# Kernel tuning notes

Measured on AMD Instinct MI355X. Metric: run time of the kernel, lower is better.

The kernel has to match this reference:

```python
import jax, jax.numpy as jnp
import numpy as np

B, T, C, H = 4, 2048, 1024, 16
HS = C // H  # head_size = 64
FF = 4 * C   # 4096
EPS = 1e-5


def _layernorm(x, g, b):
    mu = jnp.mean(x, axis=-1, keepdims=True)
    var = jnp.mean(jnp.square(x - mu), axis=-1, keepdims=True)
    return (x - mu) * jax.lax.rsqrt(var + EPS) * g + b


def setup_inputs() -> dict:
    key = jax.random.key(0)
    ks = jax.random.split(key, 12)
    s_in = 1.0 / np.sqrt(C)
    s_ff = 1.0 / np.sqrt(FF)
    return {
        "x": jax.random.normal(ks[0], (B, T, C), jnp.float32),
        # per-head projection weights stacked: [H, C, HS]
        "Wq": jax.random.normal(ks[1], (H, C, HS), jnp.float32) * s_in,
        "Wk": jax.random.normal(ks[2], (H, C, HS), jnp.float32) * s_in,
        "Wv": jax.random.normal(ks[3], (H, C, HS), jnp.float32) * s_in,
        "Wo": jax.random.normal(ks[4], (C, C), jnp.float32) * s_in,
        "bo": jnp.zeros((C,), jnp.float32),
        "g1": jnp.ones((C,), jnp.float32),
        "b1": jnp.zeros((C,), jnp.float32),
        "g2": jnp.ones((C,), jnp.float32),
        "b2": jnp.zeros((C,), jnp.float32),
        "W1": jax.random.normal(ks[5], (C, FF), jnp.float32) * s_in,
        "bf1": jnp.zeros((FF,), jnp.float32),
        "W2": jax.random.normal(ks[6], (FF, C), jnp.float32) * s_ff,
        "bf2": jnp.zeros((C,), jnp.float32),
    }


def reference(x, Wq, Wk, Wv, Wo, bo, g1, b1, g2, b2, W1, bf1, W2, bf2):
    # pre-norm
    h = _layernorm(x, g1, b1)                       # [B,T,C]
    q = jnp.einsum('btc,hcd->bhtd', h, Wq)          # [B,H,T,HS]
    k = jnp.einsum('btc,hcd->bhtd', h, Wk)
    v = jnp.einsum('btc,hcd->bhtd', h, Wv)
    w = jnp.einsum('bhtd,bhsd->bhts', q, k) * (HS ** -0.5)  # [B,H,T,S]
    mask = jnp.tril(jnp.ones((T, T), bool))          # causal tril
    w = jnp.where(mask[None, None], w, -jnp.inf)
    # NB: original code softmaxes over dim=1 of [B,T,T], i.e. the QUERY axis
    w = jax.nn.softmax(w, axis=-2)
    o = jnp.einsum('bhts,bhsd->bhtd', w, v)          # [B,H,T,HS]
    o = jnp.transpose(o, (0, 2, 1, 3)).reshape(B, T, C)  # concat heads
    x = x + o @ Wo + bo                              # residual 1 (dropout=0)
    f = _layernorm(x, g2, b2)
    ff = jax.nn.relu(f @ W1 + bf1) @ W2 + bf2        # FFN (dropout=0)
    return x + ff
```

## Files before the change

### kernel.cpp

```cpp
#include <hip/hip_runtime.h>
#include <hip/hip_bf16.h>


#define T_SEQ 2048
#define SCALE2 0.1803368801f

typedef __attribute__((ext_vector_type(8))) short short8;
typedef __attribute__((ext_vector_type(4))) float f32x4;

typedef __attribute__((address_space(1))) unsigned int g_u32;
typedef __attribute__((address_space(3))) unsigned int l_u32;

__device__ __forceinline__ unsigned short f2bf(float f) {
  __hip_bfloat16 h = __float2bfloat16(f);
  union { __hip_bfloat16 h; unsigned short u; } x; x.h = h;
  return x.u;
}
__device__ __forceinline__ float bf2f(unsigned short u) {
  union { unsigned u; float f; } x; x.u = (unsigned)u << 16;
  return x.f;
}

__device__ __forceinline__ void g2lds16(const void* g, void* l) {
  __builtin_amdgcn_global_load_lds((g_u32*)g, (l_u32*)l, 16, 0, 0);
}

__device__ __forceinline__ int xcd_swz(int flat, int nwg) {
  if ((nwg & 7) != 0) return flat;
  return (flat & 7) * (nwg >> 3) + (flat >> 3);
}

template <int EPI, int BN>
__global__ __launch_bounds__(512, 2) void gemm256(
    const unsigned short* __restrict__ A, const unsigned short* __restrict__ Bt,
    int M, int N, int K,
    unsigned short* __restrict__ out16, float* __restrict__ outF,
    const float* __restrict__ bias, const float* __restrict__ resid) {
  constexpr int WN = BN / 4;
  constexpr int FN = WN / 16;
  constexpr int NL = 4 + (BN * 8) / 512;
  extern __shared__ unsigned short lds[];
  unsigned short* ldsA = lds;
  unsigned short* ldsB = lds + 2 * 16384;
  const int tid = threadIdx.x, lane = tid & 63, wid = tid >> 6;
  const int wm = wid >> 2, wn = wid & 3;
  const int nx = gridDim.x;
  const int flat = blockIdx.y * nx + blockIdx.x;
  const int swz = xcd_swz(flat, nx * gridDim.y);
  const int mBase = (swz / nx) * 256, nBase = (swz % nx) * BN;

  f32x4 acc[8][FN];
#pragma unroll
  for (int i = 0; i < 8; ++i)
#pragma unroll
    for (int j = 0; j < FN; ++j)
#pragma unroll
      for (int e = 0; e < 4; ++e) acc[i][j][e] = 0.f;

  auto stage = [&](int buf, int kt) {
    const int k0 = kt << 6;
#pragma unroll
    for (int it = 0; it < 4; ++it) {
      int g = it * 512 + tid;
      int row = g >> 3, colL = g & 7;
      int col = colL ^ (row & 7);
      g2lds16(A + ((size_t)(mBase + row) * K + k0 + col * 8),
              &ldsA[buf * 16384 + (it * 512 + wid * 64) * 8]);
    }
#pragma unroll
    for (int it = 0; it < (BN * 8) / 512; ++it) {
      int g = it * 512 + tid;
      int row = g >> 3, colL = g & 7;
      int col = colL ^ (row & 7);
      g2lds16(Bt + ((size_t)(nBase + row) * K + k0 + col * 8),
              &ldsB[buf * (BN * 64) + (it * 512 + wid * 64) * 8]);
    }
  };

  const int nKT = K >> 6;
  stage(0, 0);
  asm volatile("s_waitcnt vmcnt(0)" ::: "memory");
  __builtin_amdgcn_sched_barrier(0);
  __builtin_amdgcn_s_barrier();
  __builtin_amdgcn_sched_barrier(0);
  if (nKT > 1) stage(1, 1);

  int cur = 0;
  for (int kt = 0; kt < nKT; ++kt) {
    short8 bf[FN][2];
#pragma unroll
    for (int fn = 0; fn < FN; ++fn)
#pragma unroll
      for (int ks = 0; ks < 2; ++ks) {
        int r = wn * WN + fn * 16 + (lane & 15);
        int c = (ks * 4 + (lane >> 4)) ^ (r & 7);
        bf[fn][ks] = *(const short8*)&ldsB[cur * (BN * 64) + r * 64 + c * 8];
      }
#pragma unroll
    for (int q = 0; q < 4; ++q) {
      short8 af[2][2];
#pragma unroll
      for (int mf = 0; mf < 2; ++mf)
#pragma unroll
        for (int ks = 0; ks < 2; ++ks) {
          int r = wm * 128 + q * 32 + mf * 16 + (lane & 15);
          int c = (ks * 4 + (lane >> 4)) ^ (r & 7);
          af[mf][ks] = *(const short8*)&ldsA[cur * 16384 + r * 64 + c * 8];
        }
      __builtin_amdgcn_s_setprio(1);
#pragma unroll
      for (int mf = 0; mf < 2; ++mf)
#pragma unroll
        for (int fn = 0; fn < FN; ++fn)
#pragma unroll
          for (int ks = 0; ks < 2; ++ks)
            acc[q * 2 + mf][fn] = __builtin_amdgcn_mfma_f32_16x16x32_bf16(
                af[mf][ks], bf[fn][ks], acc[q * 2 + mf][fn], 0, 0, 0);
      __builtin_amdgcn_s_setprio(0);
    }
    if (kt + 1 < nKT) {
      asm volatile("s_waitcnt lgkmcnt(0)" ::: "memory");
      __builtin_amdgcn_sched_barrier(0);
      __builtin_amdgcn_s_barrier();
      __builtin_amdgcn_sched_barrier(0);
      if (kt + 2 < nKT) {
        stage(cur, kt + 2);
        asm volatile("s_waitcnt vmcnt(%0)" ::"n"(NL) : "memory");
      } else {
        asm volatile("s_waitcnt vmcnt(0)" ::: "memory");
      }
      __builtin_amdgcn_sched_barrier(0);
      __builtin_amdgcn_s_barrier();
      __builtin_amdgcn_sched_barrier(0);
    }
    cur ^= 1;
  }

#pragma unroll
  for (int am = 0; am < 8; ++am)
#pragma unroll
    for (int fn = 0; fn < FN; ++fn) {
      int col = nBase + wn * WN + fn * 16 + (lane & 15);
      int row0 = mBase + wm * 128 + am * 16 + ((lane >> 4) << 2);
      if (EPI == 0) {
#pragma unroll
        for (int r = 0; r < 4; ++r)
          out16[(size_t)(row0 + r) * N + col] = f2bf(acc[am][fn][r]);
      } else if (EPI == 1) {
        float bv = bias[col];
#pragma unroll
        for (int r = 0; r < 4; ++r) {
          size_t idx = (size_t)(row0 + r) * N + col;
          outF[idx] = acc[am][fn][r] + bv + resid[idx];
        }
      } else {
        float bv = bias[col];
#pragma unroll
        for (int r = 0; r < 4; ++r)
          out16[(size_t)(row0 + r) * N + col] =
              f2bf(fmaxf(acc[am][fn][r] + bv, 0.f));
      }
    }
}

__global__ __launch_bounds__(256) void ln_bf16(
    const float* __restrict__ x, const float* __restrict__ gw,
    const float* __restrict__ bw, unsigned short* __restrict__ out) {
  __shared__ float red[8];
  const int row = blockIdx.x, tid = threadIdx.x;
  const float4 v = ((const float4*)(x + (size_t)row * 1024))[tid];
  float s = v.x + v.y + v.z + v.w;
  float q = v.x * v.x + v.y * v.y + v.z * v.z + v.w * v.w;
#pragma unroll
  for (int off = 32; off >= 1; off >>= 1) {
    s += __shfl_down(s, off);
    q += __shfl_down(q, off);
  }
  const int lane = tid & 63, wid = tid >> 6;
  if (lane == 0) { red[wid] = s; red[4 + wid] = q; }
  __syncthreads();
  float S = red[0] + red[1] + red[2] + red[3];
  float Q = red[4] + red[5] + red[6] + red[7];
  float mu = S * (1.f / 1024.f);
  float var = Q * (1.f / 1024.f) - mu * mu;
  float rs = rsqrtf(var + 1e-5f);
  int c = tid * 4;
  ushort4 ov;
  ov.x = f2bf((v.x - mu) * rs * gw[c + 0] + bw[c + 0]);
  ov.y = f2bf((v.y - mu) * rs * gw[c + 1] + bw[c + 1]);
  ov.z = f2bf((v.z - mu) * rs * gw[c + 2] + bw[c + 2]);
  ov.w = f2bf((v.w - mu) * rs * gw[c + 3] + bw[c + 3]);
  *(ushort4*)&out[(size_t)row * 1024 + c] = ov;
}

__global__ __launch_bounds__(256) void pack_qkv(
    const float* __restrict__ Wq, const float* __restrict__ Wk,
    const float* __restrict__ Wv, unsigned short* __restrict__ out) {
  __shared__ float tile[64 * 65];
  const int tid = threadIdx.x;
  const float* W = (blockIdx.z == 0) ? Wq : (blockIdx.z == 1) ? Wk : Wv;
  const int h = blockIdx.y, r0 = blockIdx.x * 64;
#pragma unroll
  for (int it = 0; it < 4; ++it) {
    int e4 = it * 256 + tid;
    int r = e4 >> 4, c4 = e4 & 15;
    float4 v = *(const float4*)&W[((size_t)h * 1024 + r0 + r) * 64 + c4 * 4];
    tile[r * 65 + c4 * 4 + 0] = v.x;
    tile[r * 65 + c4 * 4 + 1] = v.y;
    tile[r * 65 + c4 * 4 + 2] = v.z;
    tile[r * 65 + c4 * 4 + 3] = v.w;
  }
  __syncthreads();
#pragma unroll
  for (int it = 0; it < 4; ++it) {
    int e4 = it * 256 + tid;
    int d = e4 >> 4, r4 = e4 & 15;
    ushort4 ov;
    ov.x = f2bf(tile[(r4 * 4 + 0) * 65 + d]);
    ov.y = f2bf(tile[(r4 * 4 + 1) * 65 + d]);
    ov.z = f2bf(tile[(r4 * 4 + 2) * 65 + d]);
    ov.w = f2bf(tile[(r4 * 4 + 3) * 65 + d]);
    *(ushort4*)&out[(size_t)(blockIdx.z * 1024 + h * 64 + d) * 1024 + r0 +
                    r4 * 4] = ov;
  }
}

__global__ __launch_bounds__(256) void transpose_cast(
    const float* __restrict__ in, unsigned short* __restrict__ out, int R,
    int C) {
  __shared__ float tile[64 * 65];
  const int tid = threadIdx.x;
  const int r0 = blockIdx.x * 64, c0 = blockIdx.y * 64;
#pragma unroll
  for (int it = 0; it < 4; ++it) {
    int e4 = it * 256 + tid;
    int r = e4 >> 4, c4 = e4 & 15;
    float4 v = *(const float4*)&in[(size_t)(r0 + r) * C + c0 + c4 * 4];
    tile[r * 65 + c4 * 4 + 0] = v.x;
    tile[r * 65 + c4 * 4 + 1] = v.y;
    tile[r * 65 + c4 * 4 + 2] = v.z;
    tile[r * 65 + c4 * 4 + 3] = v.w;
  }
  __syncthreads();
#pragma unroll
  for (int it = 0; it < 4; ++it) {
    int e4 = it * 256 + tid;
    int c = e4 >> 4, r4 = e4 & 15;
    ushort4 ov;
    ov.x = f2bf(tile[(r4 * 4 + 0) * 65 + c]);
    ov.y = f2bf(tile[(r4 * 4 + 1) * 65 + c]);
    ov.z = f2bf(tile[(r4 * 4 + 2) * 65 + c]);
    ov.w = f2bf(tile[(r4 * 4 + 3) * 65 + c]);
    *(ushort4*)&out[(size_t)(c0 + c) * R + r0 + r4 * 4] = ov;
  }
}

__global__ __launch_bounds__(256) void vtrans(
    const unsigned short* __restrict__ qkv, const float* __restrict__ lpart,
    unsigned short* __restrict__ vT) {
  __shared__ unsigned short tile[64 * 66];
  const int tid = threadIdx.x;
  const int bh = blockIdx.y, b = bh >> 4, h = bh & 15;
  const int t0 = blockIdx.x * 64;
#pragma unroll
  for (int it = 0; it < 8; ++it) {
    int e2 = it * 256 + tid;
    int r = e2 >> 5, c2 = e2 & 31;
    unsigned v = *(const unsigned*)&qkv[(size_t)(b * T_SEQ + t0 + r) * 3072 +
                                        2048 + h * 64 + c2 * 2];
    float l0 = lpart[(size_t)bh * T_SEQ + t0 + r];
    float l1 = lpart[(size_t)(64 + bh) * T_SEQ + t0 + r];
    float li = 1.f / (l0 + l1);
    unsigned short lo = f2bf(bf2f((unsigned short)(v & 0xffff)) * li);
    unsigned short hi = f2bf(bf2f((unsigned short)(v >> 16)) * li);
    *(unsigned*)&tile[r * 66 + c2 * 2] = (unsigned)lo | ((unsigned)hi << 16);
  }
  __syncthreads();
#pragma unroll
  for (int it = 0; it < 8; ++it) {
    int e2 = it * 256 + tid;
    int d = e2 >> 5, t2 = e2 & 31;
    unsigned short a = tile[(t2 * 2) * 66 + d];
    unsigned short bb = tile[(t2 * 2 + 1) * 66 + d];
    unsigned pk = (unsigned)a | ((unsigned)bb << 16);
    *(unsigned*)&vT[(size_t)(bh * 64 + d) * T_SEQ + t0 + t2 * 2] = pk;
  }
}

__global__ __launch_bounds__(256, 4) void attn_stats(
    const unsigned short* __restrict__ qkv, float* __restrict__ lpart) {
  __shared__ unsigned short qt[4][2][32 * 64];
  __shared__ float redL[4][2][64];
  const int tid = threadIdx.x, lane = tid & 63, w = tid >> 6;
  const int f = xcd_swz(blockIdx.y * 32 + blockIdx.x, 2048);
  const int half = f & 1, px = (f >> 1) & 15, bh = f >> 5;
  const int b = bh >> 4, h = bh & 15;
  const int sxA = px, sxB = 31 - px;
  const int sA = sxA * 64, sB = sxB * 64;
  const int m = half * 4 + w;

  short8 kfA[4][2], kfB[4][2];
#pragma unroll
  for (int fn = 0; fn < 4; ++fn)
#pragma unroll
    for (int ks = 0; ks < 2; ++ks) {
      int d = 1024 + h * 64 + ks * 32 + ((lane >> 4) << 3);
      kfA[fn][ks] = *(const short8*)&qkv[(size_t)(b * T_SEQ + sA + fn * 16 +
                                                  (lane & 15)) * 3072 + d];
      kfB[fn][ks] = *(const short8*)&qkv[(size_t)(b * T_SEQ + sB + fn * 16 +
                                                  (lane & 15)) * 3072 + d];
    }
  float lA[4] = {0.f, 0.f, 0.f, 0.f}, lB[4] = {0.f, 0.f, 0.f, 0.f};

  auto stageQ = [&](int buf, int idx) {
    int t0 = idx * 32;
#pragma unroll
    for (int it = 0; it < 4; ++it) {
      int g = it * 64 + lane;
      int row = g >> 3;
      int col = (g & 7) ^ (row & 7);
      g2lds16(qkv + ((size_t)(b * T_SEQ + t0 + row) * 3072 + h * 64 + col * 8),
              &qt[w][buf][it * 512]);
    }
  };

  auto accum = [&](const short8 (&af)[2], const short8 (&kf)[4][2],
                   float (&lacc)[4], int sBase, int tRow, bool diag) {
    f32x4 sc[4];
#pragma unroll
    for (int fn = 0; fn < 4; ++fn)
#pragma unroll
      for (int e = 0; e < 4; ++e) sc[fn][e] = 0.f;
    __builtin_amdgcn_s_setprio(1);
#pragma unroll
    for (int fn = 0; fn < 4; ++fn)
#pragma unroll
      for (int ks = 0; ks < 2; ++ks)
        sc[fn] = __builtin_amdgcn_mfma_f32_16x16x32_bf16(af[ks], kf[fn][ks],
                                                         sc[fn], 0, 0, 0);
    __builtin_amdgcn_s_setprio(0);
    if (diag) {
#pragma unroll
      for (int fn = 0; fn < 4; ++fn) {
        int s = sBase + fn * 16 + (lane & 15);
        float e0 = (tRow + 0 >= s) ? exp2f(sc[fn][0] * SCALE2) : 0.f;
        float e1 = (tRow + 1 >= s) ? exp2f(sc[fn][1] * SCALE2) : 0.f;
        float e2 = (tRow + 2 >= s) ? exp2f(sc[fn][2] * SCALE2) : 0.f;
        float e3 = (tRow + 3 >= s) ? exp2f(sc[fn][3] * SCALE2) : 0.f;
        lacc[fn] += (e0 + e1) + (e2 + e3);
      }
    } else {
#pragma unroll
      for (int fn = 0; fn < 4; ++fn) {
        float e0 = exp2f(sc[fn][0] * SCALE2);
        float e1 = exp2f(sc[fn][1] * SCALE2);
        float e2 = exp2f(sc[fn][2] * SCALE2);
        float e3 = exp2f(sc[fn][3] * SCALE2);
        lacc[fn] += (e0 + e1) + (e2 + e3);
      }
    }
  };

  const int d0 = 2 * sxA - m;
  const int fi = m + (d0 > 0 ? (((d0 + 7) >> 3) << 3) : 0);
  int cur = 0;
  if (fi < 64) stageQ(0, fi);
  for (int idx = fi; idx < 64; idx += 8, cur ^= 1) {
    if (idx + 8 < 64) {
      stageQ(cur ^ 1, idx + 8);
      asm volatile("s_waitcnt vmcnt(4)" ::: "memory");
    } else {
      asm volatile("s_waitcnt vmcnt(0)" ::: "memory");
    }
    const int t0g = idx * 32;
    const bool doB = idx >= 2 * sxB;
#pragma unroll
    for (int mf = 0; mf < 2; ++mf) {
      short8 af[2];
#pragma unroll
      for (int ks = 0; ks < 2; ++ks) {
        int r = mf * 16 + (lane & 15);
        int c = (ks * 4 + (lane >> 4)) ^ (r & 7);
        af[ks] = *(const short8*)&qt[w][cur][r * 64 + c * 8];
      }
      int tRow = t0g + mf * 16 + ((lane >> 4) << 2);
      accum(af, kfA, lA, sA, tRow, idx <= 2 * sxA + 1);
      if (doB) accum(af, kfB, lB, sB, tRow, idx <= 2 * sxB + 1);
    }
  }
#pragma unroll
  for (int fn = 0; fn < 4; ++fn) {
    lA[fn] += __shfl_down(lA[fn], 32);
    lA[fn] += __shfl_down(lA[fn], 16);
    lB[fn] += __shfl_down(lB[fn], 32);
    lB[fn] += __shfl_down(lB[fn], 16);
  }
  if (lane < 16) {
#pragma unroll
    for (int fn = 0; fn < 4; ++fn) {
      redL[w][0][fn * 16 + lane] = lA[fn];
      redL[w][1][fn * 16 + lane] = lB[fn];
    }
  }
  __syncthreads();
  if (tid < 128) {
    int which = tid >> 6;
    float l = redL[0][which][lane] + redL[1][which][lane] +
              redL[2][which][lane] + redL[3][which][lane];
    int sbase = (which == 0) ? sA : sB;
    lpart[((size_t)half * 64 + bh) * T_SEQ + sbase + lane] = l;
  }
}

__global__ __launch_bounds__(256, 2) void attn_pv(
    const unsigned short* __restrict__ qkv, const unsigned short* __restrict__ vT,
    unsigned short* __restrict__ o) {
  __shared__ unsigned short kbuf[2][64 * 64];
  __shared__ unsigned short vbuf[2][64 * 64];
  __shared__ unsigned short pl[128 * 64];
  const int tid = threadIdx.x, lane = tid & 63, wid = tid >> 6;
  const int f = xcd_swz(blockIdx.y * 8 + blockIdx.x, 512);
  const int bx = f & 7, bh = f >> 3;
  const int b = bh >> 4, h = bh & 15;
  const int tA = bx * 128, tB = (15 - bx) * 128;
  const int nSTA = 2 * bx + 2, nSTB = 32 - 2 * bx;

  short8 qfA[2][2], qfB[2][2];
#pragma unroll
  for (int mf = 0; mf < 2; ++mf)
#pragma unroll
    for (int ks = 0; ks < 2; ++ks) {
      int d = h * 64 + ks * 32 + ((lane >> 4) << 3);
      int rloc = wid * 32 + mf * 16 + (lane & 15);
      qfA[mf][ks] =
          *(const short8*)&qkv[(size_t)(b * T_SEQ + tA + rloc) * 3072 + d];
      qfB[mf][ks] =
          *(const short8*)&qkv[(size_t)(b * T_SEQ + tB + rloc) * 3072 + d];
    }
  f32x4 oaccA[2][4], oaccB[2][4];
#pragma unroll
  for (int i = 0; i < 2; ++i)
#pragma unroll
    for (int j = 0; j < 4; ++j)
#pragma unroll
      for (int e = 0; e < 4; ++e) { oaccA[i][j][e] = 0.f; oaccB[i][j][e] = 0.f; }

  auto stage = [&](int buf, int st) {
#pragma unroll
    for (int it = 0; it < 2; ++it) {
      int g = it * 256 + tid;
      int row = g >> 3, colL = g & 7;
      int col = colL ^ (row & 7);
      g2lds16(qkv + ((size_t)(b * T_SEQ + st * 64 + row) * 3072 + 1024 +
                     h * 64 + col * 8),
              &kbuf[buf][(it * 256 + wid * 64) * 8]);
      g2lds16(vT + ((size_t)(bh * 64 + row) * T_SEQ + st * 64 + col * 8),
              &vbuf[buf][(it * 256 + wid * 64) * 8]);
    }
  };

  auto qkstore = [&](const short8 (&qf)[2][2], int tBase, int s0,
                     bool maskNeeded, int cur) {
    f32x4 sc[4][2];
#pragma unroll
    for (int i = 0; i < 4; ++i)
#pragma unroll
      for (int j = 0; j < 2; ++j)
#pragma unroll
        for (int e = 0; e < 4; ++e) sc[i][j][e] = 0.f;
    __builtin_amdgcn_s_setprio(1);
#pragma unroll
    for (int fn = 0; fn < 4; ++fn)
#pragma unroll
      for (int ks = 0; ks < 2; ++ks) {
        int r = fn * 16 + (lane & 15);
        int c = (ks * 4 + (lane >> 4)) ^ (r & 7);
        short8 kfr = *(const short8*)&kbuf[cur][r * 64 + c * 8];
        sc[fn][0] = __builtin_amdgcn_mfma_f32_16x16x32_bf16(kfr, qf[0][ks],
                                                            sc[fn][0], 0, 0, 0);
        sc[fn][1] = __builtin_amdgcn_mfma_f32_16x16x32_bf16(kfr, qf[1][ks],
                                                            sc[fn][1], 0, 0, 0);
      }
    __builtin_amdgcn_s_setprio(0);
#pragma unroll
    for (int mf = 0; mf < 2; ++mf) {
      int tl = wid * 32 + mf * 16 + (lane & 15);
      int tG = tBase + tl;
#pragma unroll
      for (int fn = 0; fn < 4; ++fn) {
        int sl = fn * 16 + ((lane >> 4) << 2);
        float p0 = exp2f(sc[fn][mf][0] * SCALE2);
        float p1 = exp2f(sc[fn][mf][1] * SCALE2);
        float p2 = exp2f(sc[fn][mf][2] * SCALE2);
        float p3 = exp2f(sc[fn][mf][3] * SCALE2);
        if (maskNeeded) {
          int sG = s0 + sl;
          p0 = (tG >= sG + 0) ? p0 : 0.f;
          p1 = (tG >= sG + 1) ? p1 : 0.f;
          p2 = (tG >= sG + 2) ? p2 : 0.f;
          p3 = (tG >= sG + 3) ? p3 : 0.f;
        }
        uint2 pk;
        pk.x = (unsigned)f2bf(p0) | ((unsigned)f2bf(p1) << 16);
        pk.y = (unsigned)f2bf(p2) | ((unsigned)f2bf(p3) << 16);
        int byteoff = tl * 128 + ((sl * 2) ^ ((tl & 7) << 4));
        *(uint2*)((char*)pl + byteoff) = pk;
      }
    }
  };

  auto pvphase = [&](f32x4 (&oacc)[2][4], int cur) {
    __builtin_amdgcn_s_setprio(1);
#pragma unroll
    for (int ks = 0; ks < 2; ++ks) {
      short8 pa[2];
#pragma unroll
      for (int mf = 0; mf < 2; ++mf) {
        int rowa = wid * 32 + mf * 16 + (lane & 15);
        int kb = ks * 64 + ((lane >> 4) << 4);
        pa[mf] = *(const short8*)((const char*)pl + rowa * 128 +
                                  (kb ^ ((rowa & 7) << 4)));
      }
#pragma unroll
      for (int df = 0; df < 4; ++df) {
        int r = df * 16 + (lane & 15);
        int c = (ks * 4 + (lane >> 4)) ^ (r & 7);
        short8 vb = *(const short8*)&vbuf[cur][r * 64 + c * 8];
        oacc[0][df] = __builtin_amdgcn_mfma_f32_16x16x32_bf16(pa[0], vb,
                                                              oacc[0][df], 0, 0, 0);
        oacc[1][df] = __builtin_amdgcn_mfma_f32_16x16x32_bf16(pa[1], vb,
                                                              oacc[1][df], 0, 0, 0);
      }
    }
    __builtin_amdgcn_s_setprio(0);
  };

  auto bar_lgkm = [&]() {
    asm volatile("s_waitcnt lgkmcnt(0)" ::: "memory");
    __builtin_amdgcn_sched_barrier(0);
    __builtin_amdgcn_s_barrier();
    __builtin_amdgcn_sched_barrier(0);
  };

  stage(0, 0);
  asm volatile("s_waitcnt vmcnt(0)" ::: "memory");
  __builtin_amdgcn_sched_barrier(0);
  __builtin_amdgcn_s_barrier();
  __builtin_amdgcn_sched_barrier(0);

  int cur = 0;
  for (int st = 0; st < nSTB; ++st) {
    const int s0 = st * 64;
    const bool doA = st < nSTA;

    if (st + 1 < nSTB) stage(cur ^ 1, st + 1);

    if (doA) {
      qkstore(qfA, tA, s0, st >= nSTA - 2, cur);
      bar_lgkm();
      pvphase(oaccA, cur);
      bar_lgkm();
    }
    qkstore(qfB, tB, s0, st >= nSTB - 2, cur);
    bar_lgkm();
    pvphase(oaccB, cur);
    asm volatile("s_waitcnt vmcnt(0) lgkmcnt(0)" ::: "memory");
    __builtin_amdgcn_sched_barrier(0);
    __builtin_amdgcn_s_barrier();
    __builtin_amdgcn_sched_barrier(0);
    cur ^= 1;
  }
#pragma unroll
  for (int mf = 0; mf < 2; ++mf)
#pragma unroll
    for (int df = 0; df < 4; ++df) {
      int d = h * 64 + df * 16 + (lane & 15);
      int ra = tA + wid * 32 + mf * 16 + ((lane >> 4) << 2);
      int rb = tB + wid * 32 + mf * 16 + ((lane >> 4) << 2);
#pragma unroll
      for (int r = 0; r < 4; ++r) {
        o[(size_t)(b * T_SEQ + ra + r) * 1024 + d] = f2bf(oaccA[mf][df][r]);
        o[(size_t)(b * T_SEQ + rb + r) * 1024 + d] = f2bf(oaccB[mf][df][r]);
      }
    }
}

extern "C" void kernel_launch(void* const* d_in, const int* in_sizes, int n_in,
                              void* d_out, int out_size, void* d_ws,
                              size_t ws_size, hipStream_t stream) {
  const float* x = (const float*)d_in[0];
  const float* Wq = (const float*)d_in[1];
  const float* Wk = (const float*)d_in[2];
  const float* Wv = (const float*)d_in[3];
  const float* Wo = (const float*)d_in[4];
  const float* bo = (const float*)d_in[5];
  const float* g1 = (const float*)d_in[6];
  const float* b1 = (const float*)d_in[7];
  const float* g2 = (const float*)d_in[8];
  const float* b2 = (const float*)d_in[9];
  const float* W1 = (const float*)d_in[10];
  const float* bf1 = (const float*)d_in[11];
  const float* W2 = (const float*)d_in[12];
  const float* bf2 = (const float*)d_in[13];
  float* out = (float*)d_out;

  char* ws = (char*)d_ws;
  size_t off = 0;
  auto alloc = [&](size_t bytes) {
    char* p = ws + off;
    off += (bytes + 255) & ~(size_t)255;
    return p;
  };
  unsigned short* Wqkv = (unsigned short*)alloc(3072ull * 1024 * 2);
  unsigned short* WoT = (unsigned short*)alloc(1024ull * 1024 * 2);
  unsigned short* W1T = (unsigned short*)alloc(4096ull * 1024 * 2);
  unsigned short* W2T = (unsigned short*)alloc(1024ull * 4096 * 2);
  unsigned short* hbuf = (unsigned short*)alloc(8192ull * 1024 * 2);
  char* regionE = alloc(8192ull * 3072 * 2 + 64ull * 64 * 2048 * 2);
  unsigned short* qkv = (unsigned short*)regionE;
  unsigned short* vT = (unsigned short*)(regionE + 8192ull * 3072 * 2);
  unsigned short* act = (unsigned short*)regionE;
  float* lbuf = (float*)alloc(128ull * 2048 * 4);
  float* x1 = (float*)alloc(8192ull * 1024 * 4);
  unsigned short* fbuf = (unsigned short*)alloc(8192ull * 1024 * 2);
  unsigned short* obuf = hbuf;

  (void)in_sizes; (void)n_in; (void)out_size; (void)ws_size;

  const size_t LDS128 = (2 * 16384 + 2 * 128 * 64) * 2;
  const size_t LDS256 = (2 * 16384 + 2 * 256 * 64) * 2;

  pack_qkv<<<dim3(16, 16, 3), 256, 0, stream>>>(Wq, Wk, Wv, Wqkv);
  transpose_cast<<<dim3(16, 16), 256, 0, stream>>>(Wo, WoT, 1024, 1024);
  transpose_cast<<<dim3(16, 64), 256, 0, stream>>>(W1, W1T, 1024, 4096);
  transpose_cast<<<dim3(64, 16), 256, 0, stream>>>(W2, W2T, 4096, 1024);
  ln_bf16<<<8192, 256, 0, stream>>>(x, g1, b1, hbuf);
  gemm256<0, 128><<<dim3(24, 32), 512, LDS128, stream>>>(
      hbuf, Wqkv, 8192, 3072, 1024, qkv, nullptr, nullptr, nullptr);
  attn_stats<<<dim3(32, 64), 256, 0, stream>>>(qkv, lbuf);
  vtrans<<<dim3(32, 64), 256, 0, stream>>>(qkv, lbuf, vT);
  attn_pv<<<dim3(8, 64), 256, 0, stream>>>(qkv, vT, obuf);
  gemm256<1, 128><<<dim3(8, 32), 512, LDS128, stream>>>(
      obuf, WoT, 8192, 1024, 1024, nullptr, x1, bo, x);
  ln_bf16<<<8192, 256, 0, stream>>>(x1, g2, b2, fbuf);
  gemm256<2, 256><<<dim3(16, 32), 512, LDS256, stream>>>(
      fbuf, W1T, 8192, 4096, 1024, act, nullptr, bf1, nullptr);
  gemm256<1, 128><<<dim3(8, 32), 512, LDS128, stream>>>(
      act, W2T, 8192, 1024, 4096, nullptr, out, bf2, x1);
}
```

Measured before the change: 429.1 us.

## Triple-buffer GEMM LDS pipeline and use 128-wide tiles for FFN1

Moves the GEMM K-loop from double to triple buffering, so two tiles are in flight while one is consumed, and adjusts the vmcnt waits to match. To fit the larger LDS budget, the kernel is fixed to BN=128 and the FFN up-projection drops from 256-wide to 128-wide tiles, which doubles its grid. The aim is to hide global load latency better. In exchange it uses more LDS per block (144KB), which may limit occupancy to one block per CU, and FFN1 loses A-tile reuse.

```diff
diff --git a/kernel.cpp b/kernel.cpp
--- a/kernel.cpp
+++ b/kernel.cpp
@@ -30,18 +30,19 @@
   return (flat & 7) * (nwg >> 3) + (flat >> 3);
 }
 
-template <int EPI, int BN>
+template <int EPI>
 __global__ __launch_bounds__(512, 2) void gemm256(
     const unsigned short* __restrict__ A, const unsigned short* __restrict__ Bt,
     int M, int N, int K,
     unsigned short* __restrict__ out16, float* __restrict__ outF,
     const float* __restrict__ bias, const float* __restrict__ resid) {
+  constexpr int BN = 128;
   constexpr int WN = BN / 4;
   constexpr int FN = WN / 16;
-  constexpr int NL = 4 + (BN * 8) / 512;
+  constexpr int NL = 6;
   extern __shared__ unsigned short lds[];
   unsigned short* ldsA = lds;
-  unsigned short* ldsB = lds + 2 * 16384;
+  unsigned short* ldsB = lds + 3 * 16384;
   const int tid = threadIdx.x, lane = tid & 63, wid = tid >> 6;
   const int wm = wid >> 2, wn = wid & 3;
   const int nx = gridDim.x;
@@ -68,25 +69,26 @@
               &ldsA[buf * 16384 + (it * 512 + wid * 64) * 8]);
     }
 #pragma unroll
-    for (int it = 0; it < (BN * 8) / 512; ++it) {
+    for (int it = 0; it < 2; ++it) {
       int g = it * 512 + tid;
       int row = g >> 3, colL = g & 7;
       int col = colL ^ (row & 7);
       g2lds16(Bt + ((size_t)(nBase + row) * K + k0 + col * 8),
-              &ldsB[buf * (BN * 64) + (it * 512 + wid * 64) * 8]);
+              &ldsB[buf * 8192 + (it * 512 + wid * 64) * 8]);
     }
   };
 
   const int nKT = K >> 6;
   stage(0, 0);
-  asm volatile("s_waitcnt vmcnt(0)" ::: "memory");
+  stage(1, 1);
+  stage(2, 2);
+  asm volatile("s_waitcnt vmcnt(%0)" ::"n"(2 * NL) : "memory");
   __builtin_amdgcn_sched_barrier(0);
   __builtin_amdgcn_s_barrier();
   __builtin_amdgcn_sched_barrier(0);
-  if (nKT > 1) stage(1, 1);
-
-  int cur = 0;
+
   for (int kt = 0; kt < nKT; ++kt) {
+    const int cur = kt % 3;
     short8 bf[FN][2];
 #pragma unroll
     for (int fn = 0; fn < FN; ++fn)
@@ -94,7 +96,7 @@
       for (int ks = 0; ks < 2; ++ks) {
         int r = wn * WN + fn * 16 + (lane & 15);
         int c = (ks * 4 + (lane >> 4)) ^ (r & 7);
-        bf[fn][ks] = *(const short8*)&ldsB[cur * (BN * 64) + r * 64 + c * 8];
+        bf[fn][ks] = *(const short8*)&ldsB[cur * 8192 + r * 64 + c * 8];
       }
 #pragma unroll
     for (int q = 0; q < 4; ++q) {
@@ -123,8 +125,10 @@
       __builtin_amdgcn_sched_barrier(0);
       __builtin_amdgcn_s_barrier();
       __builtin_amdgcn_sched_barrier(0);
-      if (kt + 2 < nKT) {
-        stage(cur, kt + 2);
+      if (kt + 3 < nKT) {
+        stage(cur, kt + 3);
+        asm volatile("s_waitcnt vmcnt(%0)" ::"n"(2 * NL) : "memory");
+      } else if (kt + 2 < nKT) {
         asm volatile("s_waitcnt vmcnt(%0)" ::"n"(NL) : "memory");
       } else {
         asm volatile("s_waitcnt vmcnt(0)" ::: "memory");
@@ -133,7 +137,6 @@
       __builtin_amdgcn_s_barrier();
       __builtin_amdgcn_sched_barrier(0);
     }
-    cur ^= 1;
   }
 
 #pragma unroll
@@ -627,24 +630,23 @@
 
   (void)in_sizes; (void)n_in; (void)out_size; (void)ws_size;
 
-  const size_t LDS128 = (2 * 16384 + 2 * 128 * 64) * 2;
-  const size_t LDS256 = (2 * 16384 + 2 * 256 * 64) * 2;
+  const size_t LDS3 = 3 * (16384 + 8192) * 2;
 
   pack_qkv<<<dim3(16, 16, 3), 256, 0, stream>>>(Wq, Wk, Wv, Wqkv);
   transpose_cast<<<dim3(16, 16), 256, 0, stream>>>(Wo, WoT, 1024, 1024);
   transpose_cast<<<dim3(16, 64), 256, 0, stream>>>(W1, W1T, 1024, 4096);
   transpose_cast<<<dim3(64, 16), 256, 0, stream>>>(W2, W2T, 4096, 1024);
   ln_bf16<<<8192, 256, 0, stream>>>(x, g1, b1, hbuf);
-  gemm256<0, 128><<<dim3(24, 32), 512, LDS128, stream>>>(
+  gemm256<0><<<dim3(24, 32), 512, LDS3, stream>>>(
       hbuf, Wqkv, 8192, 3072, 1024, qkv, nullptr, nullptr, nullptr);
   attn_stats<<<dim3(32, 64), 256, 0, stream>>>(qkv, lbuf);
   vtrans<<<dim3(32, 64), 256, 0, stream>>>(qkv, lbuf, vT);
   attn_pv<<<dim3(8, 64), 256, 0, stream>>>(qkv, vT, obuf);
-  gemm256<1, 128><<<dim3(8, 32), 512, LDS128, stream>>>(
+  gemm256<1><<<dim3(8, 32), 512, LDS3, stream>>>(
       obuf, WoT, 8192, 1024, 1024, nullptr, x1, bo, x);
   ln_bf16<<<8192, 256, 0, stream>>>(x1, g2, b2, fbuf);
-  gemm256<2, 256><<<dim3(16, 32), 512, LDS256, stream>>>(
+  gemm256<2><<<dim3(32, 32), 512, LDS3, stream>>>(
       fbuf, W1T, 8192, 4096, 1024, act, nullptr, bf1, nullptr);
-  gemm256<1, 128><<<dim3(8, 32), 512, LDS128, stream>>>(
+  gemm256<1><<<dim3(8, 32), 512, LDS3, stream>>>(
       act, W2T, 8192, 1024, 4096, nullptr, out, bf2, x1);
 }
```

Result: slower. 456.6 us (+6.4%).
